# Performance work log

Hardware: AMD Instinct MI355X
Metric: run time of the kernel (lower is better)

The kernel has to match this reference:

```python
import jax, jax.numpy as jnp
import numpy as np

B, T, DIN, H, DOUT = 256, 512, 128, 256, 64
LEAK = 0.01


def setup_inputs() -> dict:
    key = jax.random.key(0)
    k0, k1, k2, k3, k4, k5, k6 = jax.random.split(key, 7)
    inputs = jax.random.normal(k0, (B, T, DIN), dtype=jnp.float32)
    # original uses torch.rand(...) * sqrt(dim) for initial states
    x0 = jax.random.uniform(k1, (B, DOUT), dtype=jnp.float32) * (DOUT ** 0.5)
    h0 = jax.random.uniform(k2, (B, H), dtype=jnp.float32) * (H ** 0.5)
    # nn.Linear default init scale ~ 1/sqrt(fan_in)
    s1 = (DIN + H) ** -0.5
    s2 = H ** -0.5
    W_ih = jax.random.uniform(k3, (H, DIN + H), dtype=jnp.float32, minval=-s1, maxval=s1)
    b_ih = jax.random.uniform(k4, (H,), dtype=jnp.float32, minval=-s1, maxval=s1)
    W_ho = jax.random.uniform(k5, (DOUT, H), dtype=jnp.float32, minval=-s2, maxval=s2)
    b_ho = jax.random.uniform(k6, (DOUT,), dtype=jnp.float32, minval=-s2, maxval=s2)
    return {"inputs": inputs, "x0": x0, "h0": h0,
            "W_ih": W_ih, "b_ih": b_ih, "W_ho": W_ho, "b_ho": b_ho}


def reference(inputs, x0, h0, W_ih, b_ih, W_ho, b_ho):
    # inputs: [B, T, DIN]; scan over time with hidden state resident.
    def step(h, u_t):  # h: [B,H], u_t: [B,DIN]
        comb = jnp.concatenate([u_t, h], axis=1)           # [B, DIN+H]
        pre = comb @ W_ih.T + b_ih                          # [B, H]
        h_new = jnp.where(pre >= 0, pre, LEAK * pre)        # LeakyReLU(0.01)
        x_t = h_new @ W_ho.T + b_ho                         # [B, DOUT]
        return h_new, (x_t, h_new)

    u_seq = jnp.swapaxes(inputs, 0, 1)                      # [T, B, DIN]
    _, (xs, hs) = jax.lax.scan(step, h0, u_seq)
    # prepend initial states -> [B, T+1, *]
    x = jnp.concatenate([x0[:, None, :], jnp.swapaxes(xs, 0, 1)], axis=1)
    h = jnp.concatenate([h0[:, None, :], jnp.swapaxes(hs, 0, 1)], axis=1)
    return x, h
```

## Files before the change

kernel.cpp:

```cpp
#include <hip/hip_runtime.h>

#define BB 256
#define TT 512
#define DIN 128
#define HH 256
#define DOUT 64
#define X_ELEMS ((long)BB * 513 * DOUT)

typedef _Float16 half2_t __attribute__((ext_vector_type(2)));
typedef _Float16 half8_t __attribute__((ext_vector_type(8)));

static __device__ inline float fdot2f(half2_t a, half2_t b, float c) {
#if __has_builtin(__builtin_amdgcn_fdot2)
    return __builtin_amdgcn_fdot2(a, b, c, false);
#else
    return c + (float)a[0] * (float)b[0] + (float)a[1] * (float)b[1];
#endif
}

static __device__ inline float quad_bfly_add(float x) {
    int t = __builtin_amdgcn_mov_dpp(__float_as_int(x), 0xB1, 0xF, 0xF, true);
    x += __int_as_float(t);
    t = __builtin_amdgcn_mov_dpp(__float_as_int(x), 0x4E, 0xF, 0xF, true);
    x += __int_as_float(t);
    return x;
}

__global__ __launch_bounds__(256, 1) void rnn_fused(
        const float* __restrict__ inp, const float* __restrict__ x0,
        const float* __restrict__ h0, const float* __restrict__ W_ih,
        const float* __restrict__ b_ih, const float* __restrict__ W_ho,
        const float* __restrict__ b_ho,
        float* __restrict__ out_x, float* __restrict__ out_h) {
    __shared__ __align__(16) _Float16 hsh[2][4][72];
    __shared__ __align__(16) _Float16 ibuf[2][DIN];
    const int b = blockIdx.x;
    const int tid = threadIdx.x;
    const int g = tid >> 2, q = tid & 3;
    const int jm = tid;

    half2_t wh[4][32];
    half2_t wu[4][16];
    half2_t wo[32];
#pragma unroll
    for (int jp = 0; jp < 4; ++jp) {
        const float* wr = W_ih + (long)(4 * g + jp) * 384;
#pragma unroll
        for (int i = 0; i < 16; ++i) {
            float4 v = *(const float4*)(wr + 128 + 64 * q + 4 * i);
            wh[jp][2 * i]     = (half2_t){(_Float16)v.x, (_Float16)v.y};
            wh[jp][2 * i + 1] = (half2_t){(_Float16)v.z, (_Float16)v.w};
        }
#pragma unroll
        for (int i = 0; i < 8; ++i) {
            float4 v = *(const float4*)(wr + 32 * q + 4 * i);
            wu[jp][2 * i]     = (half2_t){(_Float16)v.x, (_Float16)v.y};
            wu[jp][2 * i + 1] = (half2_t){(_Float16)v.z, (_Float16)v.w};
        }
    }
#pragma unroll
    for (int i = 0; i < 16; ++i) {
        float4 v = *(const float4*)(W_ho + (long)g * HH + 64 * q + 4 * i);
        wo[2 * i]     = (half2_t){(_Float16)v.x, (_Float16)v.y};
        wo[2 * i + 1] = (half2_t){(_Float16)v.z, (_Float16)v.w};
    }
    const float bih_r = b_ih[jm];
    const float bho_r = b_ho[g];

    float* hrow = out_h + (long)b * 513 * HH;
    float* xrow = out_x + (long)b * 513 * DOUT;
    const float* irow = inp + (long)b * TT * DIN;

    {
        float hv0 = h0[(long)b * HH + jm];
        hrow[jm] = hv0;
        hsh[0][tid >> 6][tid & 63] = (_Float16)hv0;
    }
    if (tid < DOUT) xrow[tid] = x0[(long)b * DOUT + tid];
    float2 ipf = {0.f, 0.f};
    if (tid < 64) {
        float2 v = *(const float2*)(irow + 2 * tid);
        *(half2_t*)&ibuf[0][2 * tid] = (half2_t){(_Float16)v.x, (_Float16)v.y};
        ipf = *(const float2*)(irow + DIN + 2 * tid);
    }
    __syncthreads();

    half8_t hv[8];
    {
        const _Float16* hs = &hsh[0][q][0];
#pragma unroll
        for (int c = 0; c < 8; ++c) hv[c] = *(const half8_t*)(hs + 8 * c);
    }

    const float* ipsrc = irow + 2 * DIN + 2 * tid;
    float* hst = hrow + HH + jm;
    float* xst = xrow + DOUT + g;
    int cur = 0;
    for (int t = 0; t < TT; ++t) {
        float2 ipn = {0.f, 0.f};
        if (tid < 64 && t < TT - 2) ipn = *(const float2*)ipsrc;
        ipsrc += DIN;

        const _Float16* ib = &ibuf[t & 1][q * 32];
        half8_t uv0 = *(const half8_t*)(ib);
        half8_t uv1 = *(const half8_t*)(ib + 8);
        half8_t uv2 = *(const half8_t*)(ib + 16);
        half8_t uv3 = *(const half8_t*)(ib + 24);

        float a0 = 0.f, a1 = 0.f, a2 = 0.f, a3 = 0.f;
#pragma unroll
        for (int c = 0; c < 8; ++c) {
            half8_t hvv = hv[c];
            half2_t p0 = {hvv[0], hvv[1]}, p1 = {hvv[2], hvv[3]};
            half2_t p2 = {hvv[4], hvv[5]}, p3 = {hvv[6], hvv[7]};
            a0 = fdot2f(p0, wh[0][4 * c + 0], a0);
            a0 = fdot2f(p1, wh[0][4 * c + 1], a0);
            a0 = fdot2f(p2, wh[0][4 * c + 2], a0);
            a0 = fdot2f(p3, wh[0][4 * c + 3], a0);
            a1 = fdot2f(p0, wh[1][4 * c + 0], a1);
            a1 = fdot2f(p1, wh[1][4 * c + 1], a1);
            a1 = fdot2f(p2, wh[1][4 * c + 2], a1);
            a1 = fdot2f(p3, wh[1][4 * c + 3], a1);
            a2 = fdot2f(p0, wh[2][4 * c + 0], a2);
            a2 = fdot2f(p1, wh[2][4 * c + 1], a2);
            a2 = fdot2f(p2, wh[2][4 * c + 2], a2);
            a2 = fdot2f(p3, wh[2][4 * c + 3], a2);
            a3 = fdot2f(p0, wh[3][4 * c + 0], a3);
            a3 = fdot2f(p1, wh[3][4 * c + 1], a3);
            a3 = fdot2f(p2, wh[3][4 * c + 2], a3);
            a3 = fdot2f(p3, wh[3][4 * c + 3], a3);
        }
#define UDOT4(UV, c0)                                              \
        {                                                          \
            half2_t p0 = {UV[0], UV[1]}, p1 = {UV[2], UV[3]};      \
            half2_t p2 = {UV[4], UV[5]}, p3 = {UV[6], UV[7]};      \
            a0 = fdot2f(p0, wu[0][c0 + 0], a0);                    \
            a0 = fdot2f(p1, wu[0][c0 + 1], a0);                    \
            a0 = fdot2f(p2, wu[0][c0 + 2], a0);                    \
            a0 = fdot2f(p3, wu[0][c0 + 3], a0);                    \
            a1 = fdot2f(p0, wu[1][c0 + 0], a1);                    \
            a1 = fdot2f(p1, wu[1][c0 + 1], a1);                    \
            a1 = fdot2f(p2, wu[1][c0 + 2], a1);                    \
            a1 = fdot2f(p3, wu[1][c0 + 3], a1);                    \
            a2 = fdot2f(p0, wu[2][c0 + 0], a2);                    \
            a2 = fdot2f(p1, wu[2][c0 + 1], a2);                    \
            a2 = fdot2f(p2, wu[2][c0 + 2], a2);                    \
            a2 = fdot2f(p3, wu[2][c0 + 3], a2);                    \
            a3 = fdot2f(p0, wu[3][c0 + 0], a3);                    \
            a3 = fdot2f(p1, wu[3][c0 + 1], a3);                    \
            a3 = fdot2f(p2, wu[3][c0 + 2], a3);                    \
            a3 = fdot2f(p3, wu[3][c0 + 3], a3);                    \
        }
        UDOT4(uv0, 0)
        UDOT4(uv1, 4)
        UDOT4(uv2, 8)
        UDOT4(uv3, 12)
#undef UDOT4

        a0 = quad_bfly_add(a0);
        a1 = quad_bfly_add(a1);
        a2 = quad_bfly_add(a2);
        a3 = quad_bfly_add(a3);
        float s = (q == 0) ? a0 : (q == 1) ? a1 : (q == 2) ? a2 : a3;
        float tot = s + bih_r;
        float hn = tot >= 0.f ? tot : 0.01f * tot;
        int nxt = cur ^ 1;
        hsh[nxt][tid >> 6][tid & 63] = (_Float16)hn;
        hst[0] = hn;
        hst += HH;
        if (tid < 64 && t < TT - 1)
            *(half2_t*)&ibuf[(t + 1) & 1][2 * tid] =
                (half2_t){(_Float16)ipf.x, (_Float16)ipf.y};
        ipf = ipn;
        __syncthreads();

        const _Float16* hs = &hsh[nxt][q][0];
#pragma unroll
        for (int c = 0; c < 8; ++c) hv[c] = *(const half8_t*)(hs + 8 * c);
        float ax = 0.f;
#pragma unroll
        for (int c = 0; c < 8; ++c) {
            half8_t hvv = hv[c];
            ax = fdot2f((half2_t){hvv[0], hvv[1]}, wo[4 * c + 0], ax);
            ax = fdot2f((half2_t){hvv[2], hvv[3]}, wo[4 * c + 1], ax);
            ax = fdot2f((half2_t){hvv[4], hvv[5]}, wo[4 * c + 2], ax);
            ax = fdot2f((half2_t){hvv[6], hvv[7]}, wo[4 * c + 3], ax);
        }
        ax = quad_bfly_add(ax);
        if (q == 0) xst[0] = ax + bho_r;
        xst += DOUT;
        cur = nxt;
    }
}

extern "C" void kernel_launch(void* const* d_in, const int* in_sizes, int n_in,
                              void* d_out, int out_size, void* d_ws, size_t ws_size,
                              hipStream_t stream) {
    const float* inp  = (const float*)d_in[0];
    const float* x0   = (const float*)d_in[1];
    const float* h0   = (const float*)d_in[2];
    const float* W_ih = (const float*)d_in[3];
    const float* b_ih = (const float*)d_in[4];
    const float* W_ho = (const float*)d_in[5];
    const float* b_ho = (const float*)d_in[6];
    float* out_x = (float*)d_out;
    float* out_h = out_x + X_ELEMS;

    rnn_fused<<<dim3(256), 256, 0, stream>>>(inp, x0, h0, W_ih, b_ih, W_ho, b_ho,
                                             out_x, out_h);
}
```

Before: 584.0 us.

## Split each hidden-unit dot product across 8 lanes with 512-thread blocks

Measured after the change: 582.3 us. Within noise of the previous version (-0.3%).

```diff
diff --git a/kernel.cpp b/kernel.cpp
--- a/kernel.cpp
+++ b/kernel.cpp
@@ -26,171 +26,193 @@
     return x;
 }
 
-__global__ __launch_bounds__(256, 1) void rnn_fused(
+static __device__ inline float xor4_add(float x) {
+    int t = __builtin_amdgcn_ds_swizzle(__float_as_int(x), 0x101F);
+    return x + __int_as_float(t);
+}
+
+__global__ __launch_bounds__(512, 2) void rnn_fused(
         const float* __restrict__ inp, const float* __restrict__ x0,
         const float* __restrict__ h0, const float* __restrict__ W_ih,
         const float* __restrict__ b_ih, const float* __restrict__ W_ho,
         const float* __restrict__ b_ho,
         float* __restrict__ out_x, float* __restrict__ out_h) {
-    __shared__ __align__(16) _Float16 hsh[2][4][72];
+    __shared__ __align__(16) _Float16 hsh[2][8][40];
     __shared__ __align__(16) _Float16 ibuf[2][DIN];
     const int b = blockIdx.x;
     const int tid = threadIdx.x;
-    const int g = tid >> 2, q = tid & 3;
-    const int jm = tid;
-
-    half2_t wh[4][32];
-    half2_t wu[4][16];
-    half2_t wo[32];
+    const int g8 = tid >> 3, q8 = tid & 7, qs = q8 & 3;
+    const bool hwv = (q8 < 4);
+    const bool xwv = (q8 == 4);
+    const bool iwv = (tid < 64);
+
+    half2_t wh[4][16];
+    half2_t wu[4][8];
+    half2_t wo[16];
 #pragma unroll
     for (int jp = 0; jp < 4; ++jp) {
-        const float* wr = W_ih + (long)(4 * g + jp) * 384;
-#pragma unroll
-        for (int i = 0; i < 16; ++i) {
-            float4 v = *(const float4*)(wr + 128 + 64 * q + 4 * i);
+        const float* wr = W_ih + (long)(4 * g8 + jp) * 384;
+#pragma unroll
+        for (int i = 0; i < 8; ++i) {
+            float4 v = *(const float4*)(wr + 128 + 32 * q8 + 4 * i);
             wh[jp][2 * i]     = (half2_t){(_Float16)v.x, (_Float16)v.y};
             wh[jp][2 * i + 1] = (half2_t){(_Float16)v.z, (_Float16)v.w};
         }
 #pragma unroll
-        for (int i = 0; i < 8; ++i) {
-            float4 v = *(const float4*)(wr + 32 * q + 4 * i);
+        for (int i = 0; i < 4; ++i) {
+            float4 v = *(const float4*)(wr + 16 * q8 + 4 * i);
             wu[jp][2 * i]     = (half2_t){(_Float16)v.x, (_Float16)v.y};
             wu[jp][2 * i + 1] = (half2_t){(_Float16)v.z, (_Float16)v.w};
         }
     }
 #pragma unroll
-    for (int i = 0; i < 16; ++i) {
-        float4 v = *(const float4*)(W_ho + (long)g * HH + 64 * q + 4 * i);
+    for (int i = 0; i < 8; ++i) {
+        float4 v = *(const float4*)(W_ho + (long)g8 * HH + 32 * q8 + 4 * i);
         wo[2 * i]     = (half2_t){(_Float16)v.x, (_Float16)v.y};
         wo[2 * i + 1] = (half2_t){(_Float16)v.z, (_Float16)v.w};
     }
-    const float bih_r = b_ih[jm];
-    const float bho_r = b_ho[g];
+    const int j_own = 4 * g8 + qs;
+    const float bih = b_ih[j_own];
+    const float bho = b_ho[g8];
+
+    _Float16* hsw0 = &hsh[0][j_own >> 5][j_own & 31];
+    _Float16* hsw1 = &hsh[1][j_own >> 5][j_own & 31];
+    const _Float16* hsr0 = &hsh[0][q8][0];
+    const _Float16* hsr1 = &hsh[1][q8][0];
 
     float* hrow = out_h + (long)b * 513 * HH;
     float* xrow = out_x + (long)b * 513 * DOUT;
     const float* irow = inp + (long)b * TT * DIN;
 
-    {
-        float hv0 = h0[(long)b * HH + jm];
-        hrow[jm] = hv0;
-        hsh[0][tid >> 6][tid & 63] = (_Float16)hv0;
-    }
-    if (tid < DOUT) xrow[tid] = x0[(long)b * DOUT + tid];
+    float hprev = 0.f, xprev = 0.f;
+    if (hwv) {
+        hprev = h0[(long)b * HH + j_own];
+        *hsw0 = (_Float16)hprev;
+    }
+    if (xwv) xprev = x0[(long)b * DOUT + g8];
     float2 ipf = {0.f, 0.f};
-    if (tid < 64) {
+    if (iwv) {
         float2 v = *(const float2*)(irow + 2 * tid);
         *(half2_t*)&ibuf[0][2 * tid] = (half2_t){(_Float16)v.x, (_Float16)v.y};
         ipf = *(const float2*)(irow + DIN + 2 * tid);
     }
     __syncthreads();
 
-    half8_t hv[8];
-    {
-        const _Float16* hs = &hsh[0][q][0];
-#pragma unroll
-        for (int c = 0; c < 8; ++c) hv[c] = *(const half8_t*)(hs + 8 * c);
-    }
+    half8_t hv0 = *(const half8_t*)(hsr0);
+    half8_t hv1 = *(const half8_t*)(hsr0 + 8);
+    half8_t hv2 = *(const half8_t*)(hsr0 + 16);
+    half8_t hv3 = *(const half8_t*)(hsr0 + 24);
 
     const float* ipsrc = irow + 2 * DIN + 2 * tid;
-    float* hst = hrow + HH + jm;
-    float* xst = xrow + DOUT + g;
-    int cur = 0;
-    for (int t = 0; t < TT; ++t) {
-        float2 ipn = {0.f, 0.f};
-        if (tid < 64 && t < TT - 2) ipn = *(const float2*)ipsrc;
-        ipsrc += DIN;
-
-        const _Float16* ib = &ibuf[t & 1][q * 32];
-        half8_t uv0 = *(const half8_t*)(ib);
-        half8_t uv1 = *(const half8_t*)(ib + 8);
-        half8_t uv2 = *(const half8_t*)(ib + 16);
-        half8_t uv3 = *(const half8_t*)(ib + 24);
-
-        float a0 = 0.f, a1 = 0.f, a2 = 0.f, a3 = 0.f;
-#pragma unroll
-        for (int c = 0; c < 8; ++c) {
-            half8_t hvv = hv[c];
-            half2_t p0 = {hvv[0], hvv[1]}, p1 = {hvv[2], hvv[3]};
-            half2_t p2 = {hvv[4], hvv[5]}, p3 = {hvv[6], hvv[7]};
-            a0 = fdot2f(p0, wh[0][4 * c + 0], a0);
-            a0 = fdot2f(p1, wh[0][4 * c + 1], a0);
-            a0 = fdot2f(p2, wh[0][4 * c + 2], a0);
-            a0 = fdot2f(p3, wh[0][4 * c + 3], a0);
-            a1 = fdot2f(p0, wh[1][4 * c + 0], a1);
-            a1 = fdot2f(p1, wh[1][4 * c + 1], a1);
-            a1 = fdot2f(p2, wh[1][4 * c + 2], a1);
-            a1 = fdot2f(p3, wh[1][4 * c + 3], a1);
-            a2 = fdot2f(p0, wh[2][4 * c + 0], a2);
-            a2 = fdot2f(p1, wh[2][4 * c + 1], a2);
-            a2 = fdot2f(p2, wh[2][4 * c + 2], a2);
-            a2 = fdot2f(p3, wh[2][4 * c + 3], a2);
-            a3 = fdot2f(p0, wh[3][4 * c + 0], a3);
-            a3 = fdot2f(p1, wh[3][4 * c + 1], a3);
-            a3 = fdot2f(p2, wh[3][4 * c + 2], a3);
-            a3 = fdot2f(p3, wh[3][4 * c + 3], a3);
-        }
-#define UDOT4(UV, c0)                                              \
-        {                                                          \
-            half2_t p0 = {UV[0], UV[1]}, p1 = {UV[2], UV[3]};      \
-            half2_t p2 = {UV[4], UV[5]}, p3 = {UV[6], UV[7]};      \
-            a0 = fdot2f(p0, wu[0][c0 + 0], a0);                    \
-            a0 = fdot2f(p1, wu[0][c0 + 1], a0);                    \
-            a0 = fdot2f(p2, wu[0][c0 + 2], a0);                    \
-            a0 = fdot2f(p3, wu[0][c0 + 3], a0);                    \
-            a1 = fdot2f(p0, wu[1][c0 + 0], a1);                    \
-            a1 = fdot2f(p1, wu[1][c0 + 1], a1);                    \
-            a1 = fdot2f(p2, wu[1][c0 + 2], a1);                    \
-            a1 = fdot2f(p3, wu[1][c0 + 3], a1);                    \
-            a2 = fdot2f(p0, wu[2][c0 + 0], a2);                    \
-            a2 = fdot2f(p1, wu[2][c0 + 1], a2);                    \
-            a2 = fdot2f(p2, wu[2][c0 + 2], a2);                    \
-            a2 = fdot2f(p3, wu[2][c0 + 3], a2);                    \
-            a3 = fdot2f(p0, wu[3][c0 + 0], a3);                    \
-            a3 = fdot2f(p1, wu[3][c0 + 1], a3);                    \
-            a3 = fdot2f(p2, wu[3][c0 + 2], a3);                    \
-            a3 = fdot2f(p3, wu[3][c0 + 3], a3);                    \
-        }
-        UDOT4(uv0, 0)
-        UDOT4(uv1, 4)
-        UDOT4(uv2, 8)
-        UDOT4(uv3, 12)
-#undef UDOT4
-
-        a0 = quad_bfly_add(a0);
-        a1 = quad_bfly_add(a1);
-        a2 = quad_bfly_add(a2);
-        a3 = quad_bfly_add(a3);
-        float s = (q == 0) ? a0 : (q == 1) ? a1 : (q == 2) ? a2 : a3;
-        float tot = s + bih_r;
-        float hn = tot >= 0.f ? tot : 0.01f * tot;
-        int nxt = cur ^ 1;
-        hsh[nxt][tid >> 6][tid & 63] = (_Float16)hn;
-        hst[0] = hn;
-        hst += HH;
-        if (tid < 64 && t < TT - 1)
-            *(half2_t*)&ibuf[(t + 1) & 1][2 * tid] =
-                (half2_t){(_Float16)ipf.x, (_Float16)ipf.y};
-        ipf = ipn;
-        __syncthreads();
-
-        const _Float16* hs = &hsh[nxt][q][0];
-#pragma unroll
-        for (int c = 0; c < 8; ++c) hv[c] = *(const half8_t*)(hs + 8 * c);
-        float ax = 0.f;
-#pragma unroll
-        for (int c = 0; c < 8; ++c) {
-            half8_t hvv = hv[c];
-            ax = fdot2f((half2_t){hvv[0], hvv[1]}, wo[4 * c + 0], ax);
-            ax = fdot2f((half2_t){hvv[2], hvv[3]}, wo[4 * c + 1], ax);
-            ax = fdot2f((half2_t){hvv[4], hvv[5]}, wo[4 * c + 2], ax);
-            ax = fdot2f((half2_t){hvv[6], hvv[7]}, wo[4 * c + 3], ax);
-        }
-        ax = quad_bfly_add(ax);
-        if (q == 0) xst[0] = ax + bho_r;
-        xst += DOUT;
-        cur = nxt;
-    }
+    float* hst = hrow + j_own;
+    float* xst = xrow + g8;
+
+#define HDOT(HV, C)                                                         \
+    {                                                                       \
+        half2_t p0 = {HV[0], HV[1]}, p1 = {HV[2], HV[3]};                   \
+        half2_t p2 = {HV[4], HV[5]}, p3 = {HV[6], HV[7]};                   \
+        a0 = fdot2f(p0, wh[0][4 * (C) + 0], a0);                            \
+        a0 = fdot2f(p1, wh[0][4 * (C) + 1], a0);                            \
+        a0 = fdot2f(p2, wh[0][4 * (C) + 2], a0);                            \
+        a0 = fdot2f(p3, wh[0][4 * (C) + 3], a0);                            \
+        a1 = fdot2f(p0, wh[1][4 * (C) + 0], a1);                            \
+        a1 = fdot2f(p1, wh[1][4 * (C) + 1], a1);                            \
+        a1 = fdot2f(p2, wh[1][4 * (C) + 2], a1);                            \
+        a1 = fdot2f(p3, wh[1][4 * (C) + 3], a1);                            \
+        a2 = fdot2f(p0, wh[2][4 * (C) + 0], a2);                            \
+        a2 = fdot2f(p1, wh[2][4 * (C) + 1], a2);                            \
+        a2 = fdot2f(p2, wh[2][4 * (C) + 2], a2);                            \
+        a2 = fdot2f(p3, wh[2][4 * (C) + 3], a2);                            \
+        a3 = fdot2f(p0, wh[3][4 * (C) + 0], a3);                            \
+        a3 = fdot2f(p1, wh[3][4 * (C) + 1], a3);                            \
+        a3 = fdot2f(p2, wh[3][4 * (C) + 2], a3);                            \
+        a3 = fdot2f(p3, wh[3][4 * (C) + 3], a3);                            \
+    }
+
+#define UDOT(UV, C)                                                         \
+    {                                                                       \
+        half2_t p0 = {UV[0], UV[1]}, p1 = {UV[2], UV[3]};                   \
+        half2_t p2 = {UV[4], UV[5]}, p3 = {UV[6], UV[7]};                   \
+        a0 = fdot2f(p0, wu[0][(C) + 0], a0);                                \
+        a0 = fdot2f(p1, wu[0][(C) + 1], a0);                                \
+        a0 = fdot2f(p2, wu[0][(C) + 2], a0);                                \
+        a0 = fdot2f(p3, wu[0][(C) + 3], a0);                                \
+        a1 = fdot2f(p0, wu[1][(C) + 0], a1);                                \
+        a1 = fdot2f(p1, wu[1][(C) + 1], a1);                                \
+        a1 = fdot2f(p2, wu[1][(C) + 2], a1);                                \
+        a1 = fdot2f(p3, wu[1][(C) + 3], a1);                                \
+        a2 = fdot2f(p0, wu[2][(C) + 0], a2);                                \
+        a2 = fdot2f(p1, wu[2][(C) + 1], a2);                                \
+        a2 = fdot2f(p2, wu[2][(C) + 2], a2);                                \
+        a2 = fdot2f(p3, wu[2][(C) + 3], a2);                                \
+        a3 = fdot2f(p0, wu[3][(C) + 0], a3);                                \
+        a3 = fdot2f(p1, wu[3][(C) + 1], a3);                                \
+        a3 = fdot2f(p2, wu[3][(C) + 2], a3);                                \
+        a3 = fdot2f(p3, wu[3][(C) + 3], a3);                                \
+    }
+
+#define XDOT(HV, C)                                                         \
+    {                                                                       \
+        ax = fdot2f((half2_t){HV[0], HV[1]}, wo[4 * (C) + 0], ax);          \
+        ax = fdot2f((half2_t){HV[2], HV[3]}, wo[4 * (C) + 1], ax);          \
+        ax = fdot2f((half2_t){HV[4], HV[5]}, wo[4 * (C) + 2], ax);          \
+        ax = fdot2f((half2_t){HV[6], HV[7]}, wo[4 * (C) + 3], ax);          \
+    }
+
+#define STEP(T, PC, PN, HRD, HWD)                                           \
+    {                                                                       \
+                     \
+        if (hwv) hst[0] = hprev;                                            \
+        if (xwv) xst[0] = xprev;                                            \
+        hst += HH; xst += DOUT;                                             \
+                   \
+        float2 ipn = {0.f, 0.f};                                            \
+        if (iwv && (T) + 2 < TT) ipn = *(const float2*)ipsrc;               \
+        ipsrc += DIN;                                                       \
+                                             \
+        const _Float16* ib = &ibuf[PC][16 * q8];                            \
+        half8_t uv0 = *(const half8_t*)(ib);                                \
+        half8_t uv1 = *(const half8_t*)(ib + 8);                            \
+        float a0 = 0.f, a1 = 0.f, a2 = 0.f, a3 = 0.f;                       \
+        HDOT(hv0, 0) HDOT(hv1, 1) HDOT(hv2, 2) HDOT(hv3, 3)                 \
+        UDOT(uv0, 0) UDOT(uv1, 4)                                           \
+        a0 = quad_bfly_add(a0);                                             \
+        a1 = quad_bfly_add(a1);                                             \
+        a2 = quad_bfly_add(a2);                                             \
+        a3 = quad_bfly_add(a3);                                             \
+        float sp = (qs == 0) ? a0 : (qs == 1) ? a1 : (qs == 2) ? a2 : a3;   \
+        float s = xor4_add(sp);                                             \
+        float tot = s + bih;                                                \
+        float hn = tot >= 0.f ? tot : 0.01f * tot;                          \
+        if (hwv) *(HWD) = (_Float16)hn;                                     \
+        if (iwv) *(half2_t*)&ibuf[PN][2 * tid] =                            \
+            (half2_t){(_Float16)ipf.x, (_Float16)ipf.y};                    \
+        ipf = ipn;                                                          \
+        hprev = hn;                                                         \
+        __syncthreads();                                                    \
+              \
+        hv0 = *(const half8_t*)(HRD);                                       \
+        hv1 = *(const half8_t*)(HRD + 8);                                   \
+        hv2 = *(const half8_t*)(HRD + 16);                                  \
+        hv3 = *(const half8_t*)(HRD + 24);                                  \
+        float ax = 0.f;                                                     \
+        XDOT(hv0, 0) XDOT(hv1, 1) XDOT(hv2, 2) XDOT(hv3, 3)                 \
+        ax = quad_bfly_add(ax);                                             \
+        ax = xor4_add(ax);                                                  \
+        xprev = ax + bho;                                                   \
+    }
+
+    for (int t = 0; t < TT; t += 2) {
+        STEP(t,     0, 1, hsr1, hsw1)
+        STEP(t + 1, 1, 0, hsr0, hsw0)
+    }
+    if (hwv) hst[0] = hprev;
+    if (xwv) xst[0] = xprev;
+
+#undef STEP
+#undef HDOT
+#undef UDOT
+#undef XDOT
 }
 
 extern "C" void kernel_launch(void* const* d_in, const int* in_sizes, int n_in,
@@ -206,6 +228,6 @@
     float* out_x = (float*)d_out;
     float* out_h = out_x + X_ELEMS;
 
-    rnn_fused<<<dim3(256), 256, 0, stream>>>(inp, x0, h0, W_ih, b_ih, W_ho, b_ho,
+    rnn_fused<<<dim3(256), 512, 0, stream>>>(inp, x0, h0, W_ih, b_ih, W_ho, b_ho,
                                              out_x, out_h);
 }
```
